# Performance work log

Hardware: AMD Instinct MI355X
Metric: run time of the kernel (lower is better)

## Reference

```python
import jax, jax.numpy as jnp
import numpy as np

B, T, H, W, D, NH, DEPTH, NCODES = 2, 16, 16, 16, 512, 8, 6, 1024
HW = H * W; DH = D // NH; KH = KW = 3; SIZE = KH * KW; MLP_DIM = 2 * D
NEG = -1e9


def _ln(x, g, b, eps=1e-5):
    m = jnp.mean(x, -1, keepdims=True)
    v = jnp.mean((x - m) ** 2, -1, keepdims=True)
    return (x - m) * jax.lax.rsqrt(v + eps) * g + b


def _rope(x, pos):
    # x: [N, h, T, dh]; half-split rotary embedding
    half = x.shape[-1] // 2
    freqs = 1.0 / (10000.0 ** (jnp.arange(half, dtype=jnp.float32) / half))
    ang = pos[:, None] * freqs[None]            # [T, half]
    cos = jnp.concatenate([jnp.cos(ang), jnp.cos(ang)], -1)
    sin = jnp.concatenate([jnp.sin(ang), jnp.sin(ang)], -1)
    rot = jnp.concatenate([-x[..., half:], x[..., :half]], -1)
    return x * cos + rot * sin


def setup_inputs() -> dict:
    key = jax.random.key(0)
    keys = iter(jax.random.split(key, 64))
    def p(shape, s=0.02):
        return (s * jax.random.normal(next(keys), shape)).astype(jnp.float32)
    inp = dict(
        codes=jax.random.randint(next(keys), (B, T, HW), 0, NCODES),
        emb_table=p((NCODES, D)),
        cls_token=p((1, 1, 1, D)),
        h_emb=p((1, 1, H, D)),
        w_emb=p((1, 1, W, D)),
        emb_norm_g=jnp.ones(D), emb_norm_b=jnp.zeros(D),
        sn_g=jnp.ones((DEPTH, D)), sn_b=jnp.zeros((DEPTH, D)),
        s_wq=p((DEPTH, D, D)), s_bq=jnp.zeros((DEPTH, D)),
        s_wk=p((DEPTH, D, D)), s_bk=jnp.zeros((DEPTH, D)),
        s_wv=p((DEPTH, D, D)), s_bv=jnp.zeros((DEPTH, D)),
        s_wo=p((DEPTH, D, D)), s_bo=jnp.zeros((DEPTH, D)),
        tn_g=jnp.ones((DEPTH, D)), tn_b=jnp.zeros((DEPTH, D)),
        t_wq=p((DEPTH, D, D)), t_bq=jnp.zeros((DEPTH, D)),
        t_wk=p((DEPTH, D, D)), t_bk=jnp.zeros((DEPTH, D)),
        t_wv=p((DEPTH, D, D)), t_bv=jnp.zeros((DEPTH, D)),
        t_wo=p((DEPTH, D, D)), t_bo=jnp.zeros((DEPTH, D)),
        mn_g=jnp.ones((DEPTH, D)), mn_b=jnp.zeros((DEPTH, D)),
        mlp_w1=p((DEPTH, D, MLP_DIM)), mlp_b1=jnp.zeros((DEPTH, MLP_DIM)),
        mlp_w2=p((DEPTH, MLP_DIM, D)), mlp_b2=jnp.zeros((DEPTH, D)),
        fn_g=jnp.ones(D), fn_b=jnp.zeros(D),
    )
    return inp


def reference(codes, emb_table, cls_token, h_emb, w_emb, emb_norm_g, emb_norm_b,
              sn_g, sn_b, s_wq, s_bq, s_wk, s_bk, s_wv, s_bv, s_wo, s_bo,
              tn_g, tn_b, t_wq, t_bq, t_wk, t_bk, t_wv, t_bv, t_wo, t_bo,
              mn_g, mn_b, mlp_w1, mlp_b1, mlp_w2, mlp_b2, fn_g, fn_b):
    T1 = T + 1
    emb = emb_table[codes]                                   # [B,T,HW,D]
    # positional embeddings exactly as torch repeat / repeat_interleave
    x = emb + jnp.tile(h_emb, (1, 1, W, 1)) + jnp.repeat(w_emb, H, axis=2)
    x = jnp.concatenate([x, jnp.broadcast_to(cls_token, (B, 1, HW, D))], axis=1)
    x = _ln(x, emb_norm_g, emb_norm_b)                       # [B,T1,HW,D]

    # temporal causal mask: True = masked
    tmask = jnp.triu(jnp.ones((T1, T1), dtype=bool), 1).at[-1, -1].set(True)
    # spatial out-of-bounds mask [H,W,SIZE] from unfold of ones with zero pad
    ones_pad = jnp.pad(jnp.ones((H, W), jnp.float32), 1)
    smask = jnp.stack([ones_pad[a:a + H, b:b + W]
                       for a in range(KH) for b in range(KW)], -1) == 0

    scale = 1.0 / jnp.sqrt(jnp.float32(DH))
    pos = jnp.arange(T1, dtype=jnp.float32)
    k_list, v_list = [], []
    attn_logits = None
    for i in range(DEPTH):
        # ---- spatial windowed attention on frames 0..T-1 ----
        xg = x[:, :-1].reshape(B, T, H, W, D)
        xn = _ln(xg, sn_g[i], sn_b[i])
        pad = jnp.pad(xn, ((0, 0), (0, 0), (1, 1), (1, 1), (0, 0)))
        nb = jnp.stack([pad[:, :, a:a + H, b:b + W]
                        for a in range(KH) for b in range(KW)], axis=4)  # [B,T,H,W,SIZE,D]
        q = (xn @ s_wq[i] + s_bq[i]).reshape(B, T, H, W, NH, DH)
        kk = (nb @ s_wk[i] + s_bk[i]).reshape(B, T, H, W, SIZE, NH, DH)
        vv = (nb @ s_wv[i] + s_bv[i]).reshape(B, T, H, W, SIZE, NH, DH)
        lg = jnp.einsum('btxynd,btxysnd->btxyns', q, kk) * scale
        lg = jnp.where(smask[None, None, :, :, None, :], NEG, lg)
        a_sp = jax.nn.softmax(lg, -1)
        o = jnp.einsum('btxyns,btxysnd->btxynd', a_sp, vv).reshape(B, T, H, W, D)
        o = o @ s_wo[i] + s_bo[i]
        x_sp = (o + xg).reshape(B, T, HW, D)                 # residual (drop_path=id, eval)
        xt = jnp.concatenate([x_sp, x[:, -1:]], axis=1)      # [B,T1,HW,D]

        # ---- temporal RoPE causal attention over T1 per spatial location ----
        s = xt.transpose(0, 2, 1, 3).reshape(B * HW, T1, D)
        sn_ = _ln(s, tn_g[i], tn_b[i])
        def heads(y):
            return y.reshape(B * HW, T1, NH, DH).transpose(0, 2, 1, 3)
        qt = _rope(heads(sn_ @ t_wq[i] + t_bq[i]), pos)
        kt = _rope(heads(sn_ @ t_wk[i] + t_bk[i]), pos)
        vt = heads(sn_ @ t_wv[i] + t_bv[i])
        lt = jnp.einsum('nhqd,nhkd->nhqk', qt, kt) * scale
        lt = jnp.where(tmask[None, None], NEG, lt)
        at = jax.nn.softmax(lt, -1)
        ot = jnp.einsum('nhqk,nhkd->nhqd', at, vt).transpose(0, 2, 1, 3).reshape(B * HW, T1, D)
        s = (ot @ t_wo[i] + t_bo[i]) + s
        xo = s.reshape(B, HW, T1, D).transpose(0, 2, 1, 3)   # [B,T1,HW,D]
        # average frame 0 over HW and broadcast back (as in torch code)
        xo = xo.at[:, 0].set(jnp.broadcast_to(xo[:, 0].mean(axis=1, keepdims=True), (B, HW, D)))
        attn_logits = lt.reshape(B, HW, NH, T1, T1)

        # ---- MLP (dim -> 2*dim, tanh, -> dim), dropout off in eval ----
        y = jnp.tanh(_ln(xo, mn_g[i], mn_b[i]) @ mlp_w1[i] + mlp_b1[i]) @ mlp_w2[i] + mlp_b2[i]
        x = y + xo
        k_list.append(kt[:, :, :-1, :])
        v_list.append(vt[:, :, :-1, :])

    return _ln(x, fn_g, fn_b), attn_logits, jnp.stack(k_list), jnp.stack(v_list)
```

## Files before the change

### kernel.cpp

```cpp
#include <hip/hip_runtime.h>
#include <hip/hip_bf16.h>
#include <math.h>

#define D_    512
#define NHH   8
#define DH_   64
#define T_    16
#define T1_   17
#define HWL   256
#define B__   2
#define NEGV  -1e9f

typedef __attribute__((ext_vector_type(8))) short short8;
typedef __attribute__((ext_vector_type(4))) short short4v;
typedef __attribute__((ext_vector_type(4))) float f32x4;
typedef __hip_bfloat16 bf16;

__device__ inline float wave_sum(float v){
  #pragma unroll
  for(int o=32;o>0;o>>=1) v += __shfl_xor(v,o,64);
  return v;
}
__device__ inline float b2f(unsigned short s){
  unsigned u = ((unsigned)s)<<16; float f; __builtin_memcpy(&f,&u,4); return f;
}
__device__ inline short f2bs(float f){
  bf16 h = __float2bfloat16(f); short s; __builtin_memcpy(&s,&h,2); return s;
}
__device__ inline void gload_lds16(const void* g, void* l){
  __builtin_amdgcn_global_load_lds((const __attribute__((address_space(1))) void*)g,
                                   (__attribute__((address_space(3))) void*)l, 16, 0, 0);
}

__global__ __launch_bounds__(256) void embed_ln_kernel(
    const int* __restrict__ codes, const float* __restrict__ emb,
    const float* __restrict__ cls, const float* __restrict__ hpos,
    const float* __restrict__ wpos, const float* __restrict__ g,
    const float* __restrict__ bta, bf16* __restrict__ X){
  int row  = blockIdx.x*4 + (threadIdx.x>>6);
  int lane = threadIdx.x & 63;
  int hw = row % HWL; int bt = row / HWL; int t = bt % T1_; int bb = bt / T1_;
  float v[8];
  if(t < T_){
    int code = codes[(bb*T_ + t)*HWL + hw];
    const float4* ep = (const float4*)(emb  + (size_t)code*D_);
    const float4* hp = (const float4*)(hpos + (size_t)(hw & 15)*D_);
    const float4* wp = (const float4*)(wpos + (size_t)(hw >> 4)*D_);
    float4 a0=ep[lane*2], a1=ep[lane*2+1];
    float4 h0=hp[lane*2], h1=hp[lane*2+1];
    float4 w0=wp[lane*2], w1=wp[lane*2+1];
    v[0]=a0.x+h0.x+w0.x; v[1]=a0.y+h0.y+w0.y; v[2]=a0.z+h0.z+w0.z; v[3]=a0.w+h0.w+w0.w;
    v[4]=a1.x+h1.x+w1.x; v[5]=a1.y+h1.y+w1.y; v[6]=a1.z+h1.z+w1.z; v[7]=a1.w+h1.w+w1.w;
  } else {
    const float4* cp = (const float4*)cls;
    float4 c0=cp[lane*2], c1=cp[lane*2+1];
    v[0]=c0.x; v[1]=c0.y; v[2]=c0.z; v[3]=c0.w; v[4]=c1.x; v[5]=c1.y; v[6]=c1.z; v[7]=c1.w;
  }
  float s=0;
  #pragma unroll
  for(int j=0;j<8;j++) s += v[j];
  s = wave_sum(s);
  float mean = s*(1.f/512.f);
  float s2=0;
  #pragma unroll
  for(int j=0;j<8;j++){ float d0=v[j]-mean; s2 += d0*d0; }
  s2 = wave_sum(s2);
  float inv = rsqrtf(s2*(1.f/512.f) + 1e-5f);
  const float4* g4 = (const float4*)g; const float4* b4 = (const float4*)bta;
  float4 gv=g4[lane*2], gw=g4[lane*2+1], bv=b4[lane*2], bw=b4[lane*2+1];
  short4v r0 = { f2bs((v[0]-mean)*inv*gv.x+bv.x), f2bs((v[1]-mean)*inv*gv.y+bv.y),
                 f2bs((v[2]-mean)*inv*gv.z+bv.z), f2bs((v[3]-mean)*inv*gv.w+bv.w) };
  short4v r1 = { f2bs((v[4]-mean)*inv*gw.x+bw.x), f2bs((v[5]-mean)*inv*gw.y+bw.y),
                 f2bs((v[6]-mean)*inv*gw.z+bw.z), f2bs((v[7]-mean)*inv*gw.w+bw.w) };
  bf16* o = X + (size_t)row*D_;
  *(short4v*)&o[lane*8]     = r0;
  *(short4v*)&o[lane*8 + 4] = r1;
}

__global__ __launch_bounds__(256) void ln_kernel(
    const bf16* __restrict__ in, float* __restrict__ out,
    const float* __restrict__ g, const float* __restrict__ bta,
    int c_rpb, int s_rpb){
  int row  = blockIdx.x*4 + (threadIdx.x>>6);
  int lane = threadIdx.x & 63;
  int bb = row / c_rpb; int rem = row - bb*c_rpb;
  short8 vv = *(const short8*)(in + ((size_t)bb*s_rpb + rem)*D_ + lane*8);
  float v[8]; float s=0;
  #pragma unroll
  for(int j=0;j<8;j++){ v[j] = b2f((unsigned short)vv[j]); s += v[j]; }
  s = wave_sum(s);
  float mean = s*(1.f/512.f);
  float s2=0;
  #pragma unroll
  for(int j=0;j<8;j++){ float d0=v[j]-mean; s2 += d0*d0; }
  s2 = wave_sum(s2);
  float inv = rsqrtf(s2*(1.f/512.f) + 1e-5f);
  const float4* g4 = (const float4*)g; const float4* b4 = (const float4*)bta;
  float4 gv=g4[lane*2], gw=g4[lane*2+1], bv=b4[lane*2], bw=b4[lane*2+1];
  float4 o0 = { (v[0]-mean)*inv*gv.x+bv.x, (v[1]-mean)*inv*gv.y+bv.y,
                (v[2]-mean)*inv*gv.z+bv.z, (v[3]-mean)*inv*gv.w+bv.w };
  float4 o1 = { (v[4]-mean)*inv*gw.x+bw.x, (v[5]-mean)*inv*gw.y+bw.y,
                (v[6]-mean)*inv*gw.z+bw.z, (v[7]-mean)*inv*gw.w+bw.w };
  float* o = out + (size_t)row*D_;
  *(float4*)&o[lane*8]     = o0;
  *(float4*)&o[lane*8 + 4] = o1;
}

__global__ __launch_bounds__(256) void ln_bf_kernel(
    const bf16* __restrict__ in, bf16* __restrict__ out,
    const float* __restrict__ g, const float* __restrict__ bta,
    int c_rpb, int s_rpb){
  int row  = blockIdx.x*4 + (threadIdx.x>>6);
  int lane = threadIdx.x & 63;
  int bb = row / c_rpb; int rem = row - bb*c_rpb;
  short8 vv = *(const short8*)(in + ((size_t)bb*s_rpb + rem)*D_ + lane*8);
  float v[8]; float s=0;
  #pragma unroll
  for(int j=0;j<8;j++){ v[j] = b2f((unsigned short)vv[j]); s += v[j]; }
  s = wave_sum(s);
  float mean = s*(1.f/512.f);
  float s2=0;
  #pragma unroll
  for(int j=0;j<8;j++){ float d0=v[j]-mean; s2 += d0*d0; }
  s2 = wave_sum(s2);
  float inv = rsqrtf(s2*(1.f/512.f) + 1e-5f);
  const float4* g4 = (const float4*)g; const float4* b4 = (const float4*)bta;
  float4 gv=g4[lane*2], gw=g4[lane*2+1], bv=b4[lane*2], bw=b4[lane*2+1];
  short4v r0 = { f2bs((v[0]-mean)*inv*gv.x+bv.x), f2bs((v[1]-mean)*inv*gv.y+bv.y),
                 f2bs((v[2]-mean)*inv*gv.z+bv.z), f2bs((v[3]-mean)*inv*gv.w+bv.w) };
  short4v r1 = { f2bs((v[4]-mean)*inv*gw.x+bw.x), f2bs((v[5]-mean)*inv*gw.y+bw.y),
                 f2bs((v[6]-mean)*inv*gw.z+bw.z), f2bs((v[7]-mean)*inv*gw.w+bw.w) };
  bf16* o = out + (size_t)row*D_;
  *(short4v*)&o[lane*8]     = r0;
  *(short4v*)&o[lane*8 + 4] = r1;
}

__global__ __launch_bounds__(256) void wconv_kernel(
    const float* sq, const float* sk, const float* sv, const float* so,
    const float* tq, const float* tk, const float* tv, const float* to,
    const float* w1, const float* w2, bf16* __restrict__ dst){
  __shared__ float sm[32][33];
  int z = blockIdx.z; int i = z/10, id = z - i*10;
  const size_t wo = (size_t)i*262144, mo = (size_t)i*524288;
  bf16* db = dst + (size_t)i*3145728;
  const float* src; bf16* d; int K, N;
  switch(id){
    case 0: src=sq+wo; d=db+0*262144;  K=512;  N=512;  break;
    case 1: src=sk+wo; d=db+1*262144;  K=512;  N=512;  break;
    case 2: src=sv+wo; d=db+2*262144;  K=512;  N=512;  break;
    case 3: src=so+wo; d=db+3*262144;  K=512;  N=512;  break;
    case 4: src=tq+wo; d=db+4*262144;  K=512;  N=512;  break;
    case 5: src=tk+wo; d=db+5*262144;  K=512;  N=512;  break;
    case 6: src=tv+wo; d=db+6*262144;  K=512;  N=512;  break;
    case 7: src=to+wo; d=db+7*262144;  K=512;  N=512;  break;
    case 8: src=w1+mo; d=db+2097152;   K=512;  N=1024; break;
    default:src=w2+mo; d=db+2621440;   K=1024; N=512;  break;
  }
  int n0 = blockIdx.x<<5, k0 = blockIdx.y<<5;
  if(n0 >= N || k0 >= K) return;
  int tx = threadIdx.x & 31, ty = threadIdx.x >> 5;
  #pragma unroll
  for(int j=0;j<4;j++) sm[ty+j*8][tx] = src[(size_t)(k0+ty+j*8)*N + n0+tx];
  __syncthreads();
  #pragma unroll
  for(int j=0;j<4;j++) d[(size_t)(n0+ty+j*8)*K + k0+tx] = __float2bfloat16(sm[tx][ty+j*8]);
}

template<int ACT, bool RES>
__global__ __launch_bounds__(256) void gemm_mfma64(
    const bf16* __restrict__ A, const bf16* __restrict__ Wt,
    const float* __restrict__ bias, bf16* __restrict__ outp,
    const bf16* __restrict__ resid, int K, int N, int c_rpb, int o_rpb){
  __shared__ __align__(16) bf16 As[2][64*64];
  __shared__ __align__(16) bf16 Bs[2][64*64];
  const int tid  = threadIdx.x;
  const int lane = tid & 63;
  const int w    = tid >> 6;
  const int row0 = blockIdx.y << 6;
  const int col0 = blockIdx.x << 6;
  const int mw = (w>>1)*32, nw = (w&1)*32;
  size_t ga[2], gb[2];
  #pragma unroll
  for(int r=0;r<2;r++){
    int c = (r*4+w)*64 + lane;
    int rw = c>>3;
    int ks = (c&7) ^ (rw&7);
    ga[r] = (size_t)(row0+rw)*K + (ks<<3);
    gb[r] = (size_t)(col0+rw)*K + (ks<<3);
  }
  f32x4 acc[2][2] = {};
  #pragma unroll
  for(int r=0;r<2;r++){
    gload_lds16(A  + ga[r], &As[0][(r*4+w)*512]);
    gload_lds16(Wt + gb[r], &Bs[0][(r*4+w)*512]);
  }
  __syncthreads();
  int cur = 0;
  for(int k0=0;k0<K;k0+=64){
    if(k0+64 < K){
      #pragma unroll
      for(int r=0;r<2;r++){
        gload_lds16(A  + ga[r] + k0+64, &As[cur^1][(r*4+w)*512]);
        gload_lds16(Wt + gb[r] + k0+64, &Bs[cur^1][(r*4+w)*512]);
      }
    }
    const short8* Av = (const short8*)As[cur];
    const short8* Bv = (const short8*)Bs[cur];
    #pragma unroll
    for(int kk=0;kk<2;kk++){
      const int slot = (lane>>4) + kk*4;
      short8 af[2], bfr[2];
      #pragma unroll
      for(int mi=0;mi<2;mi++){ int rw = mw + mi*16 + (lane&15); af[mi]  = Av[rw*8 + (slot ^ (rw&7))]; }
      #pragma unroll
      for(int ni=0;ni<2;ni++){ int rw = nw + ni*16 + (lane&15); bfr[ni] = Bv[rw*8 + (slot ^ (rw&7))]; }
      #pragma unroll
      for(int mi=0;mi<2;mi++)
        #pragma unroll
        for(int ni=0;ni<2;ni++)
          acc[mi][ni] = __builtin_amdgcn_mfma_f32_16x16x32_bf16(af[mi], bfr[ni], acc[mi][ni], 0,0,0);
    }
    __syncthreads();
    cur ^= 1;
  }
  #pragma unroll
  for(int mi=0;mi<2;mi++){
    #pragma unroll
    for(int r=0;r<4;r++){
      int row = row0 + mw + mi*16 + (lane>>4)*4 + r;
      int bb = row / c_rpb;
      size_t orow = (size_t)bb*o_rpb + (row - bb*c_rpb);
      #pragma unroll
      for(int ni=0;ni<2;ni++){
        int col = col0 + nw + ni*16 + (lane&15);
        float v = acc[mi][ni][r] + bias[col];
        if(ACT==1) v = tanhf(v);
        if(RES) v += __bfloat162float(resid[orow*(size_t)N + col]);
        outp[orow*(size_t)N + col] = __float2bfloat16(v);
      }
    }
  }
}

__global__ __launch_bounds__(256) void gemm_qkv(
    const bf16* __restrict__ A, const bf16* __restrict__ Wt,
    const float* __restrict__ bq, const float* __restrict__ bk, const float* __restrict__ bv,
    bf16* __restrict__ Qo, bf16* __restrict__ Ko, bf16* __restrict__ Vo){
  const int K = 512;
  __shared__ __align__(16) bf16 As[128*64];
  __shared__ __align__(16) bf16 Bs[128*64];
  const int tid  = threadIdx.x;
  const int lane = tid & 63;
  const int w    = tid >> 6;
  const int row0 = blockIdx.y << 7;
  const int col0 = blockIdx.x << 7;
  const int mb = (w>>1)*64, nb = (w&1)*64;
  size_t ga[4], gb[4];
  #pragma unroll
  for(int r=0;r<4;r++){
    int c = (r*4+w)*64 + lane;
    int rw = c>>3;
    int ks = (c&7) ^ (rw&7);
    ga[r] = (size_t)(row0+rw)*K + (ks<<3);
    gb[r] = (size_t)(col0+rw)*K + (ks<<3);
  }
  f32x4 acc[4][4] = {};
  for(int k0=0;k0<K;k0+=64){
    #pragma unroll
    for(int r=0;r<4;r++){
      gload_lds16(A  + ga[r] + k0, As + (size_t)(r*4+w)*512);
      gload_lds16(Wt + gb[r] + k0, Bs + (size_t)(r*4+w)*512);
    }
    __syncthreads();
    const short8* Av = (const short8*)As;
    const short8* Bv = (const short8*)Bs;
    #pragma unroll
    for(int kk=0;kk<2;kk++){
      const int slot = (lane>>4) + kk*4;
      short8 af[4], bfr[4];
      #pragma unroll
      for(int mi=0;mi<4;mi++){ int rw = mb + mi*16 + (lane&15); af[mi]  = Av[rw*8 + (slot ^ (rw&7))]; }
      #pragma unroll
      for(int ni=0;ni<4;ni++){ int rw = nb + ni*16 + (lane&15); bfr[ni] = Bv[rw*8 + (slot ^ (rw&7))]; }
      #pragma unroll
      for(int mi=0;mi<4;mi++)
        #pragma unroll
        for(int ni=0;ni<4;ni++)
          acc[mi][ni] = __builtin_amdgcn_mfma_f32_16x16x32_bf16(af[mi], bfr[ni], acc[mi][ni], 0,0,0);
    }
    __syncthreads();
  }
  const int sel = col0 >> 9;
  bf16* outp = (sel==0) ? Qo : (sel==1 ? Ko : Vo);
  const float* bp = (sel==0) ? bq : (sel==1 ? bk : bv);
  const int cb = col0 & 511;
  #pragma unroll
  for(int mi=0;mi<4;mi++){
    #pragma unroll
    for(int r=0;r<4;r++){
      int row = row0 + mb + mi*16 + (lane>>4)*4 + r;
      #pragma unroll
      for(int ni=0;ni<4;ni++){
        int col = cb + nb + ni*16 + (lane&15);
        outp[(size_t)row*512 + col] = __float2bfloat16(acc[mi][ni][r] + bp[col]);
      }
    }
  }
}

__global__ __launch_bounds__(256) void spatial_attn_kernel(
    const bf16* __restrict__ Q, const bf16* __restrict__ K,
    const bf16* __restrict__ V, bf16* __restrict__ O){
  int loc = blockIdx.x;
  int hw = loc & 255;
  int hh = hw >> 4, ww = hw & 15;
  int tid = threadIdx.x, lane = tid & 63, w = tid >> 6;
  int h = w*2 + (lane>>5);
  int j = lane & 31;
  size_t base = (size_t)loc*D_ + h*DH_ + 2*j;
  unsigned uq = *(const unsigned*)&Q[base];
  float q0 = b2f((unsigned short)uq), q1 = b2f((unsigned short)(uq>>16));
  float lg[9]; int nrow[9];
  #pragma unroll
  for(int s=0;s<9;s++){
    int a = s/3 - 1, b2_ = s%3 - 1;
    int nh = hh + a, nw = ww + b2_;
    bool ok = ((unsigned)nh < 16u) && ((unsigned)nw < 16u);
    nrow[s] = ok ? (loc - hw + (nh<<4) + nw) : -1;
    float p = 0.f;
    if(ok){
      unsigned uk = *(const unsigned*)&K[(size_t)nrow[s]*D_ + h*DH_ + 2*j];
      p = q0*b2f((unsigned short)uk) + q1*b2f((unsigned short)(uk>>16));
    }
    #pragma unroll
    for(int o=16;o>0;o>>=1) p += __shfl_xor(p, o, 64);
    lg[s] = ok ? p*0.125f : NEGV;
  }
  float m = lg[0];
  #pragma unroll
  for(int s=1;s<9;s++) m = fmaxf(m, lg[s]);
  float den = 0.f, wv[9];
  #pragma unroll
  for(int s=0;s<9;s++){ wv[s] = __expf(lg[s]-m); den += wv[s]; }
  float inv = 1.f/den;
  float a0 = 0.f, a1 = 0.f;
  #pragma unroll
  for(int s=0;s<9;s++){
    if(nrow[s] >= 0){
      unsigned uv = *(const unsigned*)&V[(size_t)nrow[s]*D_ + h*DH_ + 2*j];
      a0 += wv[s]*b2f((unsigned short)uv);
      a1 += wv[s]*b2f((unsigned short)(uv>>16));
    }
  }
  unsigned up = (unsigned)(unsigned short)f2bs(a0*inv) | ((unsigned)(unsigned short)f2bs(a1*inv) << 16);
  *(unsigned*)&O[base] = up;
}

__global__ __launch_bounds__(512) void fused_tattn(
    const bf16* __restrict__ Qb, const bf16* __restrict__ Kb, const bf16* __restrict__ Vb,
    bf16* __restrict__ O, float* __restrict__ kout, float* __restrict__ vout,
    float* __restrict__ ltout, int write_lt){
  __shared__ __align__(16) bf16 Qs[17*520];
  __shared__ __align__(16) bf16 Ks[17*520];
  __shared__ __align__(16) bf16 Vs[17*512];
  __shared__ float Ws[8][17][18];
  const int tid = threadIdx.x, w = tid>>6, lane = tid&63;
  const int hw = blockIdx.x & 255, b = blockIdx.x >> 8;
  const size_t tstr = (size_t)HWL*D_;
  const size_t rb0 = ((size_t)(b*T1_)*HWL + hw)*D_;
  for(int t=w; t<17; t+=8){
    size_t src = rb0 + (size_t)t*tstr + lane*8;
    *(short8*)&Qs[t*520 + lane*8] = *(const short8*)&Qb[src];
    *(short8*)&Ks[t*520 + lane*8] = *(const short8*)&Kb[src];
    *(short8*)&Vs[t*512 + lane*8] = *(const short8*)&Vb[src];
  }
  __syncthreads();
  {
    int i = lane & 31;
    float freq = __expf(-9.210340372f * (float)i * (1.f/32.f));
    bf16* P = (lane < 32) ? Qs : Ks;
    #pragma unroll
    for(int t=0;t<17;t++){
      float sn, cs; __sincosf((float)t*freq, &sn, &cs);
      int idx = t*520 + w*64 + i;
      float x1 = __bfloat162float(P[idx]);
      float x2 = __bfloat162float(P[idx+32]);
      P[idx]    = __float2bfloat16(x1*cs - x2*sn);
      P[idx+32] = __float2bfloat16(x2*cs + x1*sn);
    }
  }
  __syncthreads();
  {
    size_t eb = (((size_t)(b*HWL + hw)*NHH + w)*16)*64 + lane;
    #pragma unroll
    for(int t=0;t<16;t++){
      kout[eb + t*64] = __bfloat162float(Ks[t*520 + w*64 + lane]);
      vout[eb + t*64] = __bfloat162float(Vs[t*512 + w*64 + lane]);
    }
  }
  size_t lb = ((size_t)(b*HWL + hw)*NHH + w)*289;
  for(int p=lane; p<289; p+=64){
    int t = p/17, u = p - t*17;
    float d = 0.f;
    #pragma unroll
    for(int jj=0;jj<8;jj++){
      short8 qq = *(short8*)&Qs[t*520 + w*64 + jj*8];
      short8 kk = *(short8*)&Ks[u*520 + w*64 + jj*8];
      #pragma unroll
      for(int e=0;e<8;e++) d += b2f((unsigned short)qq[e]) * b2f((unsigned short)kk[e]);
    }
    bool masked = (u > t) || (t == 16 && u == 16);
    float lg = masked ? NEGV : d*0.125f;
    Ws[w][t][u] = lg;
    if(write_lt) ltout[lb + t*17 + u] = lg;
  }
  __syncthreads();
  if(lane < 17){
    float m = -1e30f;
    #pragma unroll
    for(int u=0;u<17;u++) m = fmaxf(m, Ws[w][lane][u]);
    float den = 0.f, e[17];
    #pragma unroll
    for(int u=0;u<17;u++){ e[u] = __expf(Ws[w][lane][u]-m); den += e[u]; }
    float inv = 1.f/den;
    #pragma unroll
    for(int u=0;u<17;u++) Ws[w][lane][u] = e[u]*inv;
  }
  __syncthreads();
  float Vr[17];
  #pragma unroll
  for(int u=0;u<17;u++) Vr[u] = __bfloat162float(Vs[u*512 + w*64 + lane]);
  #pragma unroll
  for(int t=0;t<17;t++){
    float acc = 0.f;
    #pragma unroll
    for(int u=0;u<17;u++) acc += Ws[w][t][u]*Vr[u];
    O[rb0 + (size_t)t*tstr + w*64 + lane] = __float2bfloat16(acc);
  }
}

__global__ __launch_bounds__(256) void avg_frame0_kernel(bf16* __restrict__ X){
  int b = blockIdx.x >> 3, c = blockIdx.x & 7;
  int ro = threadIdx.x >> 6, dd = threadIdx.x & 63;
  size_t base = ((size_t)(b*T1_)*HWL)*D_ + c*64 + dd;
  float acc = 0.f;
  for(int r=ro; r<256; r+=4) acc += __bfloat162float(X[base + (size_t)r*D_]);
  __shared__ float sm[4][64];
  sm[ro][dd] = acc;
  __syncthreads();
  float v = (sm[0][dd]+sm[1][dd]+sm[2][dd]+sm[3][dd])*(1.f/256.f);
  bf16 bv = __float2bfloat16(v);
  for(int r=ro; r<256; r+=4) X[base + (size_t)r*D_] = bv;
}

extern "C" void kernel_launch(void* const* d_in, const int* in_sizes, int n_in,
                              void* d_out, int out_size, void* d_ws, size_t ws_size,
                              hipStream_t stream){
  const int*   codes = (const int*)  d_in[0];
  const float* emb   = (const float*)d_in[1];
  const float* cls   = (const float*)d_in[2];
  const float* hpos  = (const float*)d_in[3];
  const float* wpos  = (const float*)d_in[4];
  const float* eng   = (const float*)d_in[5];
  const float* enb   = (const float*)d_in[6];
  const float* sn_g  = (const float*)d_in[7];
  const float* sn_b  = (const float*)d_in[8];
  const float* s_wq  = (const float*)d_in[9];
  const float* s_bq  = (const float*)d_in[10];
  const float* s_wk  = (const float*)d_in[11];
  const float* s_bk  = (const float*)d_in[12];
  const float* s_wv  = (const float*)d_in[13];
  const float* s_bv  = (const float*)d_in[14];
  const float* s_wo  = (const float*)d_in[15];
  const float* s_bo  = (const float*)d_in[16];
  const float* tn_g  = (const float*)d_in[17];
  const float* tn_b  = (const float*)d_in[18];
  const float* t_wq  = (const float*)d_in[19];
  const float* t_bq  = (const float*)d_in[20];
  const float* t_wk  = (const float*)d_in[21];
  const float* t_bk  = (const float*)d_in[22];
  const float* t_wv  = (const float*)d_in[23];
  const float* t_bv  = (const float*)d_in[24];
  const float* t_wo  = (const float*)d_in[25];
  const float* t_bo  = (const float*)d_in[26];
  const float* mn_g  = (const float*)d_in[27];
  const float* mn_b  = (const float*)d_in[28];
  const float* mw1   = (const float*)d_in[29];
  const float* mb1   = (const float*)d_in[30];
  const float* mw2   = (const float*)d_in[31];
  const float* mb2   = (const float*)d_in[32];
  const float* fn_g  = (const float*)d_in[33];
  const float* fn_b  = (const float*)d_in[34];

  const size_t NX = 4456448;
  bf16* Xb  = (bf16*)d_ws;
  bf16* XNb = Xb  + NX;
  bf16* Qb  = XNb + NX;
  bf16* Kb  = Qb  + NX;
  bf16* Vb  = Kb  + NX;
  bf16* Wt  = Vb  + NX;
  bf16* HIDb= Qb;

  float* out0 = (float*)d_out;
  float* out1 = out0 + NX;
  float* out2 = out1 + 1183744;
  float* out3 = out2 + 25165824;

  const int RS = B__*T_*HWL;
  const int RT = B__*T1_*HWL;
  dim3 gQs(12, 64);
  dim3 gQt(12, 68);
  dim3 g64s(8, 128);
  dim3 g64t(8, 136);
  dim3 gM1(16, 136);
  dim3 wcg(32, 32, 60);

  embed_ln_kernel<<<RT/4, 256, 0, stream>>>(codes, emb, cls, hpos, wpos, eng, enb, Xb);
  wconv_kernel<<<wcg,256,0,stream>>>(s_wq, s_wk, s_wv, s_wo, t_wq, t_wk, t_wv, t_wo, mw1, mw2, Wt);

  for(int i=0;i<6;i++){
    bf16* Wl = Wt + (size_t)i*3145728;
    ln_bf_kernel<<<RS/4,256,0,stream>>>(Xb, XNb, sn_g+i*D_, sn_b+i*D_, T_*HWL, T1_*HWL);
    gemm_qkv<<<gQs,256,0,stream>>>(XNb, Wl, s_bq+i*D_, s_bk+i*D_, s_bv+i*D_, Qb, Kb, Vb);
    spatial_attn_kernel<<<RS,256,0,stream>>>(Qb, Kb, Vb, XNb);
    gemm_mfma64<0,true><<<g64s,256,0,stream>>>(XNb, Wl+3*262144, s_bo+i*D_, Xb, Xb, 512, 512, T_*HWL, T1_*HWL);
    ln_bf_kernel<<<RT/4,256,0,stream>>>(Xb, XNb, tn_g+i*D_, tn_b+i*D_, T1_*HWL, T1_*HWL);
    gemm_qkv<<<gQt,256,0,stream>>>(XNb, Wl+4*262144, t_bq+i*D_, t_bk+i*D_, t_bv+i*D_, Qb, Kb, Vb);
    fused_tattn<<<512,512,0,stream>>>(Qb, Kb, Vb, XNb,
                                      out2+(size_t)i*4194304, out3+(size_t)i*4194304,
                                      out1, (i==5)?1:0);
    gemm_mfma64<0,true><<<g64t,256,0,stream>>>(XNb, Wl+7*262144, t_bo+i*D_, Xb, Xb, 512, 512, RT, RT);
    avg_frame0_kernel<<<16,256,0,stream>>>(Xb);
    ln_bf_kernel<<<RT/4,256,0,stream>>>(Xb, XNb, mn_g+i*D_, mn_b+i*D_, T1_*HWL, T1_*HWL);
    gemm_mfma64<1,false><<<gM1,256,0,stream>>>(XNb, Wl+2097152, mb1+i*1024, HIDb, nullptr, 512, 1024, RT, RT);
    gemm_mfma64<0,true><<<g64t,256,0,stream>>>(HIDb, Wl+2621440, mb2+i*D_, Xb, Xb, 1024, 512, RT, RT);
  }
  ln_kernel<<<RT/4,256,0,stream>>>(Xb, out0, fn_g, fn_b, T1_*HWL, T1_*HWL);
}
```

Measured before the change: 1.385 ms.

## Use triple-buffered 8-wave 256x128 GEMM for QKV and MLP up-projection

```diff
diff --git a/kernel.cpp b/kernel.cpp
--- a/kernel.cpp
+++ b/kernel.cpp
@@ -166,6 +166,147 @@
   for(int j=0;j<4;j++) d[(size_t)(n0+ty+j*8)*K + k0+tx] = __float2bfloat16(sm[tx][ty+j*8]);
 }
 
+template<int MODE>
+__global__ __launch_bounds__(512) void gemm_8p(
+    const bf16* __restrict__ A, const bf16* __restrict__ Wt,
+    const float* __restrict__ b0, const float* __restrict__ b1, const float* __restrict__ b2,
+    bf16* __restrict__ o0, bf16* __restrict__ o1, bf16* __restrict__ o2,
+    int K, int N){
+  __shared__ __align__(16) bf16 As[3][256*64];
+  __shared__ __align__(16) bf16 Bs[3][128*64];
+  const int tid  = threadIdx.x;
+  const int lane = tid & 63;
+  const int w    = tid >> 6;
+  const int wr   = w >> 1;
+  const int wc   = w & 1;
+  const int row0 = blockIdx.y << 8;
+  const int col0 = blockIdx.x << 7;
+
+  size_t gA[4], gB[2];
+  #pragma unroll
+  for(int j=0;j<4;j++){
+    int c = tid + j*512; int rw = c>>3; int ks = (c&7) ^ (rw&7);
+    gA[j] = (size_t)(row0+rw)*K + (ks<<3);
+  }
+  #pragma unroll
+  for(int j=0;j<2;j++){
+    int c = tid + j*512; int rw = c>>3; int ks = (c&7) ^ (rw&7);
+    gB[j] = (size_t)(col0+rw)*K + (ks<<3);
+  }
+
+  const int NT = K >> 6;
+  #pragma unroll
+  for(int tt=0; tt<2; ++tt){
+    #pragma unroll
+    for(int j=0;j<4;j++) gload_lds16(A  + gA[j] + tt*64, &As[tt][(size_t)(tid + j*512)*8]);
+    #pragma unroll
+    for(int j=0;j<2;j++) gload_lds16(Wt + gB[j] + tt*64, &Bs[tt][(size_t)(tid + j*512)*8]);
+  }
+  asm volatile("s_waitcnt vmcnt(6)" ::: "memory");
+  __builtin_amdgcn_s_barrier();
+  __builtin_amdgcn_sched_barrier(0);
+
+  f32x4 acc[4][4] = {};
+  for(int t=0; t<NT; ++t){
+    const short8* Av = (const short8*)As[t%3];
+    const short8* Bv = (const short8*)Bs[t%3];
+    bf16* An = As[(t+2)%3];
+    bf16* Bn = Bs[(t+2)%3];
+    const bool pf = (t+2 < NT);
+    const int kn = (t+2) << 6;
+    if(pf){
+      gload_lds16(A  + gA[0] + kn, &An[(size_t)tid*8]);
+      gload_lds16(A  + gA[1] + kn, &An[(size_t)(tid+512)*8]);
+      gload_lds16(Wt + gB[0] + kn, &Bn[(size_t)tid*8]);
+    }
+    short8 bfr[4][2], af01[2][2];
+    #pragma unroll
+    for(int ni=0;ni<4;ni++)
+      #pragma unroll
+      for(int kk=0;kk<2;kk++){
+        int rw2 = wc*64 + ni*16 + (lane&15);
+        int s = (lane>>4) + kk*4;
+        bfr[ni][kk] = Bv[rw2*8 + (s ^ (rw2&7))];
+      }
+    #pragma unroll
+    for(int mi=0;mi<2;mi++)
+      #pragma unroll
+      for(int kk=0;kk<2;kk++){
+        int rw2 = wr*64 + mi*16 + (lane&15);
+        int s = (lane>>4) + kk*4;
+        af01[mi][kk] = Av[rw2*8 + (s ^ (rw2&7))];
+      }
+    __builtin_amdgcn_s_setprio(1);
+    #pragma unroll
+    for(int mi=0;mi<2;mi++)
+      #pragma unroll
+      for(int ni=0;ni<4;ni++)
+        #pragma unroll
+        for(int kk=0;kk<2;kk++)
+          acc[mi][ni] = __builtin_amdgcn_mfma_f32_16x16x32_bf16(af01[mi][kk], bfr[ni][kk], acc[mi][ni], 0,0,0);
+    __builtin_amdgcn_s_setprio(0);
+    if(pf){
+      gload_lds16(A  + gA[2] + kn, &An[(size_t)(tid+1024)*8]);
+      gload_lds16(A  + gA[3] + kn, &An[(size_t)(tid+1536)*8]);
+      gload_lds16(Wt + gB[1] + kn, &Bn[(size_t)(tid+512)*8]);
+    }
+    short8 af23[2][2];
+    #pragma unroll
+    for(int mi=0;mi<2;mi++)
+      #pragma unroll
+      for(int kk=0;kk<2;kk++){
+        int rw2 = wr*64 + (mi+2)*16 + (lane&15);
+        int s = (lane>>4) + kk*4;
+        af23[mi][kk] = Av[rw2*8 + (s ^ (rw2&7))];
+      }
+    __builtin_amdgcn_s_setprio(1);
+    #pragma unroll
+    for(int mi=0;mi<2;mi++)
+      #pragma unroll
+      for(int ni=0;ni<4;ni++)
+        #pragma unroll
+        for(int kk=0;kk<2;kk++)
+          acc[mi+2][ni] = __builtin_amdgcn_mfma_f32_16x16x32_bf16(af23[mi][kk], bfr[ni][kk], acc[mi+2][ni], 0,0,0);
+    __builtin_amdgcn_s_setprio(0);
+    if(t < NT-1){
+      if(pf) asm volatile("s_waitcnt vmcnt(6)" ::: "memory");
+      else   asm volatile("s_waitcnt vmcnt(0)" ::: "memory");
+      __builtin_amdgcn_s_barrier();
+      __builtin_amdgcn_sched_barrier(0);
+    }
+  }
+  if(MODE == 1){
+    const int sel = col0 >> 9;
+    bf16* outp = (sel==0) ? o0 : (sel==1 ? o1 : o2);
+    const float* bp = (sel==0) ? b0 : (sel==1 ? b1 : b2);
+    const int cb = (col0 & 511) + wc*64;
+    #pragma unroll
+    for(int mi=0;mi<4;mi++)
+      #pragma unroll
+      for(int r=0;r<4;r++){
+        int row = row0 + wr*64 + mi*16 + (lane>>4)*4 + r;
+        #pragma unroll
+        for(int ni=0;ni<4;ni++){
+          int col = cb + ni*16 + (lane&15);
+          outp[(size_t)row*512 + col] = __float2bfloat16(acc[mi][ni][r] + bp[col]);
+        }
+      }
+  } else {
+    #pragma unroll
+    for(int mi=0;mi<4;mi++)
+      #pragma unroll
+      for(int r=0;r<4;r++){
+        int row = row0 + wr*64 + mi*16 + (lane>>4)*4 + r;
+        #pragma unroll
+        for(int ni=0;ni<4;ni++){
+          int col = col0 + wc*64 + ni*16 + (lane&15);
+          float v = tanhf(acc[mi][ni][r] + b0[col]);
+          o0[(size_t)row*N + col] = __float2bfloat16(v);
+        }
+      }
+  }
+}
+
 template<int ACT, bool RES>
 __global__ __launch_bounds__(256) void gemm_mfma64(
     const bf16* __restrict__ A, const bf16* __restrict__ Wt,
@@ -237,72 +378,6 @@
         if(ACT==1) v = tanhf(v);
         if(RES) v += __bfloat162float(resid[orow*(size_t)N + col]);
         outp[orow*(size_t)N + col] = __float2bfloat16(v);
-      }
-    }
-  }
-}
-
-__global__ __launch_bounds__(256) void gemm_qkv(
-    const bf16* __restrict__ A, const bf16* __restrict__ Wt,
-    const float* __restrict__ bq, const float* __restrict__ bk, const float* __restrict__ bv,
-    bf16* __restrict__ Qo, bf16* __restrict__ Ko, bf16* __restrict__ Vo){
-  const int K = 512;
-  __shared__ __align__(16) bf16 As[128*64];
-  __shared__ __align__(16) bf16 Bs[128*64];
-  const int tid  = threadIdx.x;
-  const int lane = tid & 63;
-  const int w    = tid >> 6;
-  const int row0 = blockIdx.y << 7;
-  const int col0 = blockIdx.x << 7;
-  const int mb = (w>>1)*64, nb = (w&1)*64;
-  size_t ga[4], gb[4];
-  #pragma unroll
-  for(int r=0;r<4;r++){
-    int c = (r*4+w)*64 + lane;
-    int rw = c>>3;
-    int ks = (c&7) ^ (rw&7);
-    ga[r] = (size_t)(row0+rw)*K + (ks<<3);
-    gb[r] = (size_t)(col0+rw)*K + (ks<<3);
-  }
-  f32x4 acc[4][4] = {};
-  for(int k0=0;k0<K;k0+=64){
-    #pragma unroll
-    for(int r=0;r<4;r++){
-      gload_lds16(A  + ga[r] + k0, As + (size_t)(r*4+w)*512);
-      gload_lds16(Wt + gb[r] + k0, Bs + (size_t)(r*4+w)*512);
-    }
-    __syncthreads();
-    const short8* Av = (const short8*)As;
-    const short8* Bv = (const short8*)Bs;
-    #pragma unroll
-    for(int kk=0;kk<2;kk++){
-      const int slot = (lane>>4) + kk*4;
-      short8 af[4], bfr[4];
-      #pragma unroll
-      for(int mi=0;mi<4;mi++){ int rw = mb + mi*16 + (lane&15); af[mi]  = Av[rw*8 + (slot ^ (rw&7))]; }
-      #pragma unroll
-      for(int ni=0;ni<4;ni++){ int rw = nb + ni*16 + (lane&15); bfr[ni] = Bv[rw*8 + (slot ^ (rw&7))]; }
-      #pragma unroll
-      for(int mi=0;mi<4;mi++)
-        #pragma unroll
-        for(int ni=0;ni<4;ni++)
-          acc[mi][ni] = __builtin_amdgcn_mfma_f32_16x16x32_bf16(af[mi], bfr[ni], acc[mi][ni], 0,0,0);
-    }
-    __syncthreads();
-  }
-  const int sel = col0 >> 9;
-  bf16* outp = (sel==0) ? Qo : (sel==1 ? Ko : Vo);
-  const float* bp = (sel==0) ? bq : (sel==1 ? bk : bv);
-  const int cb = col0 & 511;
-  #pragma unroll
-  for(int mi=0;mi<4;mi++){
-    #pragma unroll
-    for(int r=0;r<4;r++){
-      int row = row0 + mb + mi*16 + (lane>>4)*4 + r;
-      #pragma unroll
-      for(int ni=0;ni<4;ni++){
-        int col = cb + nb + ni*16 + (lane&15);
-        outp[(size_t)row*512 + col] = __float2bfloat16(acc[mi][ni][r] + bp[col]);
       }
     }
   }
@@ -508,11 +583,11 @@
 
   const int RS = B__*T_*HWL;
   const int RT = B__*T1_*HWL;
-  dim3 gQs(12, 64);
-  dim3 gQt(12, 68);
+  dim3 gQs8(12, 32);
+  dim3 gQt8(12, 34);
+  dim3 gM18(8, 34);
   dim3 g64s(8, 128);
   dim3 g64t(8, 136);
-  dim3 gM1(16, 136);
   dim3 wcg(32, 32, 60);
 
   embed_ln_kernel<<<RT/4, 256, 0, stream>>>(codes, emb, cls, hpos, wpos, eng, enb, Xb);
@@ -521,18 +596,21 @@
   for(int i=0;i<6;i++){
     bf16* Wl = Wt + (size_t)i*3145728;
     ln_bf_kernel<<<RS/4,256,0,stream>>>(Xb, XNb, sn_g+i*D_, sn_b+i*D_, T_*HWL, T1_*HWL);
-    gemm_qkv<<<gQs,256,0,stream>>>(XNb, Wl, s_bq+i*D_, s_bk+i*D_, s_bv+i*D_, Qb, Kb, Vb);
+    gemm_8p<1><<<gQs8,512,0,stream>>>(XNb, Wl, s_bq+i*D_, s_bk+i*D_, s_bv+i*D_,
+                                      Qb, Kb, Vb, 512, 1536);
     spatial_attn_kernel<<<RS,256,0,stream>>>(Qb, Kb, Vb, XNb);
     gemm_mfma64<0,true><<<g64s,256,0,stream>>>(XNb, Wl+3*262144, s_bo+i*D_, Xb, Xb, 512, 512, T_*HWL, T1_*HWL);
     ln_bf_kernel<<<RT/4,256,0,stream>>>(Xb, XNb, tn_g+i*D_, tn_b+i*D_, T1_*HWL, T1_*HWL);
-    gemm_qkv<<<gQt,256,0,stream>>>(XNb, Wl+4*262144, t_bq+i*D_, t_bk+i*D_, t_bv+i*D_, Qb, Kb, Vb);
+    gemm_8p<1><<<gQt8,512,0,stream>>>(XNb, Wl+4*262144, t_bq+i*D_, t_bk+i*D_, t_bv+i*D_,
+                                      Qb, Kb, Vb, 512, 1536);
     fused_tattn<<<512,512,0,stream>>>(Qb, Kb, Vb, XNb,
                                       out2+(size_t)i*4194304, out3+(size_t)i*4194304,
                                       out1, (i==5)?1:0);
     gemm_mfma64<0,true><<<g64t,256,0,stream>>>(XNb, Wl+7*262144, t_bo+i*D_, Xb, Xb, 512, 512, RT, RT);
     avg_frame0_kernel<<<16,256,0,stream>>>(Xb);
     ln_bf_kernel<<<RT/4,256,0,stream>>>(Xb, XNb, mn_g+i*D_, mn_b+i*D_, T1_*HWL, T1_*HWL);
-    gemm_mfma64<1,false><<<gM1,256,0,stream>>>(XNb, Wl+2097152, mb1+i*1024, HIDb, nullptr, 512, 1024, RT, RT);
+    gemm_8p<0><<<gM18,512,0,stream>>>(XNb, Wl+2097152, mb1+i*1024, nullptr, nullptr,
+                                      HIDb, nullptr, nullptr, 512, 1024);
     gemm_mfma64<0,true><<<g64t,256,0,stream>>>(HIDb, Wl+2621440, mb2+i*D_, Xb, Xb, 1024, 512, RT, RT);
   }
   ln_kernel<<<RT/4,256,0,stream>>>(Xb, out0, fn_g, fn_b, T1_*HWL, T1_*HWL);
```

After: 1.524 ms. 1.1x slower.
